# Kernel optimization log

Measured on AMD Instinct MI355X. Metric: run time of the kernel, lower is better.

## Reference

```python
import jax, jax.numpy as jnp
import numpy as np
import math

N_EMBD = 512
N_HEAD = 8
B, T = 2, 4096


def setup_inputs() -> dict:
    key = jax.random.key(0)
    ks = jax.random.split(key, 12)
    s = 1.0 / math.sqrt(N_EMBD)
    inp = {
        "x": jax.random.normal(ks[0], (B, T, N_EMBD), dtype=jnp.float32),
        "weight": jax.random.uniform(ks[1], (1,), dtype=jnp.float32),
        "state": jax.random.uniform(ks[2], (1,), dtype=jnp.float32),
        "Wq": jax.random.normal(ks[3], (N_EMBD, N_EMBD), dtype=jnp.float32) * s,
        "bq": jnp.zeros((N_EMBD,), dtype=jnp.float32),
        "Wk": jax.random.normal(ks[4], (N_EMBD, N_EMBD), dtype=jnp.float32) * s,
        "bk": jnp.zeros((N_EMBD,), dtype=jnp.float32),
        "Wv": jax.random.normal(ks[5], (N_EMBD, N_EMBD), dtype=jnp.float32) * s,
        "bv": jnp.zeros((N_EMBD,), dtype=jnp.float32),
        "Wp": jax.random.normal(ks[6], (N_EMBD, N_EMBD), dtype=jnp.float32) * s,
        "bp": jnp.zeros((N_EMBD,), dtype=jnp.float32),
    }
    return inp


def reference(x, weight, state, Wq, bq, Wk, bk, Wv, bv, Wp, bp):
    # weight / state are accepted but unused, matching the torch module.
    Bb, Tt, C = x.shape
    hd = C // N_HEAD

    def split_heads(t):  # [B,T,C] -> [B,H,T,hd]
        return t.reshape(Bb, Tt, N_HEAD, hd).transpose(0, 2, 1, 3)

    # torch nn.Linear: y = x @ W.T + b
    q = split_heads(x @ Wq.T + bq)
    k = split_heads(x @ Wk.T + bk)
    v = split_heads(x @ Wv.T + bv)

    scale = 1.0 / math.sqrt(hd)
    att = jnp.einsum("bhqd,bhkd->bhqk", q, k) * scale  # [B,H,T,T]
    causal = jnp.tril(jnp.ones((Tt, Tt), dtype=bool))
    att = jnp.where(causal[None, None, :, :], att, -jnp.inf)
    att = jax.nn.softmax(att, axis=-1)
    # attn_drop / resid_drop are identity (p=0 / eval)
    y = jnp.einsum("bhqk,bhkd->bhqd", att, v)  # [B,H,T,hd]
    y = y.transpose(0, 2, 1, 3).reshape(Bb, Tt, C)
    return y @ Wp.T + bp
```

## Files before the change

### kernel.cpp

```cpp
#include <hip/hip_runtime.h>
#include <math.h>

using short8  = __attribute__((ext_vector_type(8))) short;
using floatx4 = __attribute__((ext_vector_type(4))) float;

#define DEVI __device__ __forceinline__

#define BATCH 2
#define SEQ   4096
#define NE    512
#define NH    8
#define HD    64
#define MTOT  8192

#define QSCALE 0.18033688011112042f

DEVI short f2bf(float f) {
    unsigned u = __builtin_bit_cast(unsigned, f);
    unsigned r = (u + 0x7fffu + ((u >> 16) & 1u)) >> 16;
    return (short)r;
}

DEVI void async16(const void* g, void* l) {
    __builtin_amdgcn_global_load_lds(
        (const __attribute__((address_space(1))) void*)g,
        (__attribute__((address_space(3))) void*)l, 16, 0, 0);
}

__global__ __launch_bounds__(256) void cvt_all(const float* __restrict__ x,
                                               const float* __restrict__ wq,
                                               const float* __restrict__ wk,
                                               const float* __restrict__ wv,
                                               const float* __restrict__ wp,
                                               short* __restrict__ xbf,
                                               short* __restrict__ wbf) {
    int i = blockIdx.x * 256 + threadIdx.x;
    const float* src; short* dst; int off;
    if (i < MTOT * NE / 4) {
        src = x; dst = xbf; off = i;
    } else {
        int j = i - MTOT * NE / 4;
        int wsel = j >> 16;
        off = j & 65535;
        src = (wsel == 0) ? wq : (wsel == 1) ? wk : (wsel == 2) ? wv : wp;
        dst = wbf + (size_t)wsel * NE * NE;
    }
    float4 f = ((const float4*)src)[off];
    short4 o;
    o.x = f2bf(f.x); o.y = f2bf(f.y); o.z = f2bf(f.z); o.w = f2bf(f.w);
    ((short4*)dst)[off] = o;
}

DEVI void gemm_mainloop(const short* __restrict__ A, const short* __restrict__ W,
                        int m0, int n0, short* ldsA, short* ldsW, floatx4 (&acc)[4][4]) {
    const int tid  = threadIdx.x;
    const int lane = tid & 63;
    const int w    = tid >> 6;
    const int wm   = w >> 1, wn = w & 1;
    const int quad = lane >> 4, l15 = lane & 15;
    const int srow = lane >> 3, scol = (lane & 7) * 8;

    for (int i = 0; i < 4; ++i)
        for (int j = 0; j < 4; ++j)
            acc[i][j] = floatx4{0.f, 0.f, 0.f, 0.f};

    for (int kt = 0; kt < NE / 64; ++kt) {
        const int k0 = kt * 64;
        for (int c = 0; c < 4; ++c) {
            const int rb = w * 32 + c * 8;
            async16(A + (size_t)(m0 + rb + srow) * NE + k0 + scol, ldsA + rb * 64);
            async16(W + (size_t)(n0 + rb + srow) * NE + k0 + scol, ldsW + rb * 64);
        }
        __syncthreads();
        for (int ks = 0; ks < 2; ++ks) {
            short8 af[4], bf[4];
            for (int i = 0; i < 4; ++i)
                af[i] = *(const short8*)(ldsA + (wm * 64 + i * 16 + l15) * 64 + ks * 32 + quad * 8);
            for (int j = 0; j < 4; ++j)
                bf[j] = *(const short8*)(ldsW + (wn * 64 + j * 16 + l15) * 64 + ks * 32 + quad * 8);
            for (int i = 0; i < 4; ++i)
                for (int j = 0; j < 4; ++j)
                    acc[i][j] = __builtin_amdgcn_mfma_f32_16x16x32_bf16(af[i], bf[j], acc[i][j], 0, 0, 0);
        }
        __syncthreads();
    }
}

__global__ __launch_bounds__(256) void gemm_qkv(const short* __restrict__ xbf,
                                                const short* __restrict__ wbf,
                                                const float* __restrict__ bq,
                                                const float* __restrict__ bk,
                                                const float* __restrict__ bv,
                                                short* __restrict__ qkv) {
    __shared__ short ldsA[128 * 64];
    __shared__ short ldsW[128 * 64];
    const int m0 = blockIdx.x * 128, n0 = blockIdx.y * 128, z = blockIdx.z;
    const short* W = wbf + (size_t)z * (NE * NE);
    const float* bias = (z == 0) ? bq : (z == 1) ? bk : bv;
    short* out = qkv + (size_t)z * (MTOT * NE);

    floatx4 acc[4][4];
    gemm_mainloop(xbf, W, m0, n0, ldsA, ldsW, acc);

    const int lane = threadIdx.x & 63, w = threadIdx.x >> 6;
    const int wm = w >> 1, wn = w & 1, quad = lane >> 4, l15 = lane & 15;
    const float scale = (z == 0) ? QSCALE : 1.0f;
    for (int j = 0; j < 4; ++j) {
        const int col = n0 + wn * 64 + j * 16 + l15;
        const float bz = bias[col];
        const int h = col >> 6, d = col & 63;
        for (int i = 0; i < 4; ++i) {
            for (int r = 0; r < 4; ++r) {
                const int row = m0 + wm * 64 + i * 16 + quad * 4 + r;
                const int b = row >> 12, t = row & 4095;
                const float v = (acc[i][j][r] + bz) * scale;
                out[(((size_t)(b * NH + h)) * SEQ + t) * HD + d] = f2bf(v);
            }
        }
    }
}

__global__ __launch_bounds__(256) void transpose_v(const short* __restrict__ vb,
                                                   short* __restrict__ vt) {
    const int bh = blockIdx.y;
    const int t0 = blockIdx.x * 64;
    __shared__ short tile[64 * 66];
    const int tid = threadIdx.x;
    const int r  = tid >> 3;
    const int c8 = tid & 7;

    const short* src = vb + ((size_t)bh * SEQ + t0) * HD;
#pragma unroll
    for (int p = 0; p < 2; ++p) {
        const int row = p * 32 + r;
        short8 v = *(const short8*)&src[row * HD + c8 * 8];
#pragma unroll
        for (int i = 0; i < 8; ++i)
            tile[row * 66 + c8 * 8 + i] = v[i];
    }
    __syncthreads();

    short* dst = vt + (size_t)bh * (HD * SEQ) + t0;
#pragma unroll
    for (int p = 0; p < 2; ++p) {
        const int d = p * 32 + r;
        short8 o;
#pragma unroll
        for (int i = 0; i < 8; ++i)
            o[i] = tile[(c8 * 8 + i) * 66 + d];
        *(short8*)&dst[(size_t)d * SEQ + c8 * 8] = o;
    }
}

__global__ __launch_bounds__(256) void gemm_proj(const short* __restrict__ ybf,
                                                 const short* __restrict__ wp,
                                                 const float* __restrict__ bp,
                                                 float* __restrict__ out) {
    __shared__ short ldsA[128 * 64];
    __shared__ short ldsW[128 * 64];
    const int m0 = blockIdx.x * 128, n0 = blockIdx.y * 128;

    floatx4 acc[4][4];
    gemm_mainloop(ybf, wp, m0, n0, ldsA, ldsW, acc);

    const int lane = threadIdx.x & 63, w = threadIdx.x >> 6;
    const int wm = w >> 1, wn = w & 1, quad = lane >> 4, l15 = lane & 15;
    for (int j = 0; j < 4; ++j) {
        const int col = n0 + wn * 64 + j * 16 + l15;
        const float bz = bp[col];
        for (int i = 0; i < 4; ++i) {
            for (int r = 0; r < 4; ++r) {
                const int row = m0 + wm * 64 + i * 16 + quad * 4 + r;
                out[(size_t)row * NE + col] = acc[i][j][r] + bz;
            }
        }
    }
}

template<bool DOMASK>
DEVI void attn_subtile(const short* __restrict__ bK, const short* __restrict__ bV,
                       const short8 (&qfrag)[2], short* __restrict__ myP,
                       floatx4 (&O)[4], float (&lsum)[4],
                       const int p0, const int p1, const int quad, const int l15,
                       const int w) {
    short8 kf[2][4], vf[2][4];
#pragma unroll
    for (int n = 0; n < 4; ++n) {
        const int row = n * 16 + l15;
        kf[0][n] = *(const short8*)(bK + row * 64 + p0 * 8);
        kf[1][n] = *(const short8*)(bK + row * 64 + p1 * 8);
        vf[0][n] = *(const short8*)(bV + row * 64 + p0 * 8);
        vf[1][n] = *(const short8*)(bV + row * 64 + p1 * 8);
    }

    floatx4 S[4];
#pragma unroll
    for (int n = 0; n < 4; ++n) S[n] = floatx4{0.f, 0.f, 0.f, 0.f};
    __builtin_amdgcn_s_setprio(1);
#pragma unroll
    for (int ks = 0; ks < 2; ++ks)
#pragma unroll
        for (int n = 0; n < 4; ++n)
            S[n] = __builtin_amdgcn_mfma_f32_16x16x32_bf16(qfrag[ks], kf[ks][n], S[n], 0, 0, 0);
    __builtin_amdgcn_s_setprio(0);

    if (DOMASK) {
#pragma unroll
        for (int n = 0; n < 4; ++n)
#pragma unroll
            for (int r = 0; r < 4; ++r) {
                const int rowl = w * 16 + quad * 4 + r;
                const int coll = n * 16 + l15;
                if (coll > rowl) S[n][r] = -3.0e38f;
            }
    }

#pragma unroll
    for (int n = 0; n < 4; ++n)
#pragma unroll
        for (int r = 0; r < 4; ++r)
            S[n][r] = __builtin_amdgcn_exp2f(S[n][r]);
#pragma unroll
    for (int r = 0; r < 4; ++r)
        lsum[r] += (S[0][r] + S[1][r]) + (S[2][r] + S[3][r]);

#pragma unroll
    for (int n = 0; n < 4; ++n)
#pragma unroll
        for (int r = 0; r < 4; ++r)
            myP[(quad * 4 + r) * 72 + n * 16 + l15] = f2bf(S[n][r]);

    short8 pf[2];
#pragma unroll
    for (int ks = 0; ks < 2; ++ks)
        pf[ks] = *(const short8*)(myP + l15 * 72 + ks * 32 + quad * 8);

    __builtin_amdgcn_s_setprio(1);
#pragma unroll
    for (int ks = 0; ks < 2; ++ks)
#pragma unroll
        for (int n = 0; n < 4; ++n)
            O[n] = __builtin_amdgcn_mfma_f32_16x16x32_bf16(pf[ks], vf[ks][n], O[n], 0, 0, 0);
    __builtin_amdgcn_s_setprio(0);
}

__global__ __launch_bounds__(256, 2) void attn(const short* __restrict__ q,
                                               const short* __restrict__ k,
                                               const short* __restrict__ vt,
                                               short* __restrict__ y) {
    const int id = blockIdx.x;
    const int bx = id >> 4;
    const int bh = ((id & 7) << 1) | ((id >> 3) & 1);
    const int tid = threadIdx.x, lane = tid & 63, w = tid >> 6;
    const int quad = lane >> 4, l15 = lane & 15;

    __shared__ short ldsK[2][2][64 * 64];
    __shared__ short ldsV[2][2][64 * 64];
    __shared__ short ldsP[4][16 * 72];

    const short* K  = k  + (size_t)bh * (SEQ * HD);
    const short* VT = vt + (size_t)bh * (HD * SEQ);
    short* myP = (short*)ldsP[w];
    const int b = bh >> 3, h = bh & 7;

    const int lb   = ((lane & 7) - (lane >> 3)) & 7;
    const int jrow = lane >> 3;
    const int p0 = (quad + (l15 & 7)) & 7;
    const int p1 = p0 ^ 4;

    for (int sel = 0; sel < 2; ++sel) {
        const int qt = sel ? (SEQ / 64 - 1 - bx) : bx;
        const short* Q = q + (size_t)bh * (SEQ * HD) + (size_t)qt * 64 * HD;

        short8 qfrag[2];
#pragma unroll
        for (int ks = 0; ks < 2; ++ks)
            qfrag[ks] = *(const short8*)&Q[(w * 16 + l15) * HD + ks * 32 + quad * 8];

        floatx4 O[4];
        float lsum[4];
#pragma unroll
        for (int n = 0; n < 4; ++n) O[n] = floatx4{0.f, 0.f, 0.f, 0.f};
#pragma unroll
        for (int r = 0; r < 4; ++r) lsum[r] = 0.f;

        const int npair = (qt >> 1) + 1;

        __syncthreads();
#pragma unroll
        for (int s = 0; s < 2; ++s) {
            const short* Kt = K + (size_t)s * 64 * HD;
            const short* Vc = VT + s * 64;
#pragma unroll
            for (int c2 = 0; c2 < 2; ++c2) {
                const int chunk = w * 2 + c2;
                const int j = chunk * 8 + jrow;
                async16(Kt + (size_t)j * HD + lb * 8, ldsK[0][s] + chunk * 512);
                async16(Vc + (size_t)j * SEQ + lb * 8, ldsV[0][s] + chunk * 512);
            }
        }

        for (int p = 0; p + 1 < npair; ++p) {
            __syncthreads();
            const int pipe = p & 1, nx = pipe ^ 1;

#pragma unroll
            for (int s = 0; s < 2; ++s) {
                const int js = 2 * (p + 1) + s;
                const short* Kt = K + (size_t)js * 64 * HD;
                const short* Vc = VT + js * 64;
#pragma unroll
                for (int c2 = 0; c2 < 2; ++c2) {
                    const int chunk = w * 2 + c2;
                    const int j = chunk * 8 + jrow;
                    async16(Kt + (size_t)j * HD + lb * 8, ldsK[nx][s] + chunk * 512);
                    async16(Vc + (size_t)j * SEQ + lb * 8, ldsV[nx][s] + chunk * 512);
                }
            }

            attn_subtile<false>(ldsK[pipe][0], ldsV[pipe][0], qfrag, myP, O, lsum,
                                p0, p1, quad, l15, w);
            attn_subtile<false>(ldsK[pipe][1], ldsV[pipe][1], qfrag, myP, O, lsum,
                                p0, p1, quad, l15, w);
        }

        {
            __syncthreads();
            const int ep = (npair - 1) & 1;
            if (qt & 1) {
                attn_subtile<false>(ldsK[ep][0], ldsV[ep][0], qfrag, myP, O, lsum,
                                    p0, p1, quad, l15, w);
                attn_subtile<true >(ldsK[ep][1], ldsV[ep][1], qfrag, myP, O, lsum,
                                    p0, p1, quad, l15, w);
            } else {
                attn_subtile<true >(ldsK[ep][0], ldsV[ep][0], qfrag, myP, O, lsum,
                                    p0, p1, quad, l15, w);
            }
        }

#pragma unroll
        for (int r = 0; r < 4; ++r) {
#pragma unroll
            for (int off = 1; off < 16; off <<= 1)
                lsum[r] += __shfl_xor(lsum[r], off, 64);
        }

#pragma unroll
        for (int r = 0; r < 4; ++r) {
            const float inv = 1.0f / lsum[r];
            const int t = qt * 64 + w * 16 + quad * 4 + r;
#pragma unroll
            for (int n = 0; n < 4; ++n) {
                const int col = h * 64 + n * 16 + l15;
                y[((size_t)(b * SEQ + t)) * NE + col] = f2bf(O[n][r] * inv);
            }
        }
    }
}

extern "C" void kernel_launch(void* const* d_in, const int* in_sizes, int n_in,
                              void* d_out, int out_size, void* d_ws, size_t ws_size,
                              hipStream_t stream) {
    const float* x  = (const float*)d_in[0];
    const float* Wq = (const float*)d_in[3];
    const float* bq = (const float*)d_in[4];
    const float* Wk = (const float*)d_in[5];
    const float* bk = (const float*)d_in[6];
    const float* Wv = (const float*)d_in[7];
    const float* bv = (const float*)d_in[8];
    const float* Wp = (const float*)d_in[9];
    const float* bp = (const float*)d_in[10];
    float* out = (float*)d_out;

    short* ws   = (short*)d_ws;
    short* xbf  = ws;
    short* wbf  = xbf + (size_t)MTOT * NE;
    short* qb   = wbf + 4 * (size_t)NE * NE;
    short* kb   = qb + (size_t)MTOT * NE;
    short* vb   = kb + (size_t)MTOT * NE;
    short* vtb  = xbf;
    short* yb   = vb;

    cvt_all<<<dim3((MTOT * NE / 4 + 4 * NE * NE / 4) / 256), 256, 0, stream>>>(
        x, Wq, Wk, Wv, Wp, xbf, wbf);

    gemm_qkv<<<dim3(MTOT / 128, NE / 128, 3), 256, 0, stream>>>(xbf, wbf, bq, bk, bv, qb);

    transpose_v<<<dim3(SEQ / 64, BATCH * NH), 256, 0, stream>>>(vb, vtb);

    attn<<<dim3(512), 256, 0, stream>>>(qb, kb, vtb, yb);

    gemm_proj<<<dim3(MTOT / 128, NE / 128), 256, 0, stream>>>(yb, wbf + 3 * (size_t)NE * NE, bp, out);
}
```

Before: 204.0 us.

## Split attention work into one q-tile per block and read V directly from global

The attention kernel now launches one block per query tile (1024 blocks, longest tiles first) instead of pairing a short and long tile per block. V fragments are loaded straight from global memory rather than staged through LDS, which halves the shared-memory footprint and allows raising launch bounds to 3 blocks per CU. The aim is higher occupancy and better load balance, at the cost of uncoalesced, unpipelined global V loads and losing the explicit pairing balance.

```diff
diff --git a/kernel.cpp b/kernel.cpp
--- a/kernel.cpp
+++ b/kernel.cpp
@@ -178,19 +178,24 @@
 }
 
 template<bool DOMASK>
-DEVI void attn_subtile(const short* __restrict__ bK, const short* __restrict__ bV,
+DEVI void attn_subtile(const short* __restrict__ bK, const short* __restrict__ Vg,
                        const short8 (&qfrag)[2], short* __restrict__ myP,
                        floatx4 (&O)[4], float (&lsum)[4],
                        const int p0, const int p1, const int quad, const int l15,
                        const int w) {
-    short8 kf[2][4], vf[2][4];
+    short8 vf[2][4];
+#pragma unroll
+    for (int ks = 0; ks < 2; ++ks)
+#pragma unroll
+        for (int n = 0; n < 4; ++n)
+            vf[ks][n] = *(const short8*)&Vg[(size_t)(n * 16 + l15) * SEQ + ks * 32 + quad * 8];
+
+    short8 kf[2][4];
 #pragma unroll
     for (int n = 0; n < 4; ++n) {
         const int row = n * 16 + l15;
         kf[0][n] = *(const short8*)(bK + row * 64 + p0 * 8);
         kf[1][n] = *(const short8*)(bK + row * 64 + p1 * 8);
-        vf[0][n] = *(const short8*)(bV + row * 64 + p0 * 8);
-        vf[1][n] = *(const short8*)(bV + row * 64 + p1 * 8);
     }
 
     floatx4 S[4];
@@ -244,18 +249,17 @@
     __builtin_amdgcn_s_setprio(0);
 }
 
-__global__ __launch_bounds__(256, 2) void attn(const short* __restrict__ q,
+__global__ __launch_bounds__(256, 3) void attn(const short* __restrict__ q,
                                                const short* __restrict__ k,
                                                const short* __restrict__ vt,
                                                short* __restrict__ y) {
     const int id = blockIdx.x;
-    const int bx = id >> 4;
+    const int qt = 63 - (id >> 4);
     const int bh = ((id & 7) << 1) | ((id >> 3) & 1);
     const int tid = threadIdx.x, lane = tid & 63, w = tid >> 6;
     const int quad = lane >> 4, l15 = lane & 15;
 
     __shared__ short ldsK[2][2][64 * 64];
-    __shared__ short ldsV[2][2][64 * 64];
     __shared__ short ldsP[4][16 * 72];
 
     const short* K  = k  + (size_t)bh * (SEQ * HD);
@@ -268,92 +272,84 @@
     const int p0 = (quad + (l15 & 7)) & 7;
     const int p1 = p0 ^ 4;
 
-    for (int sel = 0; sel < 2; ++sel) {
-        const int qt = sel ? (SEQ / 64 - 1 - bx) : bx;
-        const short* Q = q + (size_t)bh * (SEQ * HD) + (size_t)qt * 64 * HD;
-
-        short8 qfrag[2];
-#pragma unroll
-        for (int ks = 0; ks < 2; ++ks)
-            qfrag[ks] = *(const short8*)&Q[(w * 16 + l15) * HD + ks * 32 + quad * 8];
-
-        floatx4 O[4];
-        float lsum[4];
-#pragma unroll
-        for (int n = 0; n < 4; ++n) O[n] = floatx4{0.f, 0.f, 0.f, 0.f};
-#pragma unroll
-        for (int r = 0; r < 4; ++r) lsum[r] = 0.f;
-
-        const int npair = (qt >> 1) + 1;
-
+    const short* Q = q + (size_t)bh * (SEQ * HD) + (size_t)qt * 64 * HD;
+
+    short8 qfrag[2];
+#pragma unroll
+    for (int ks = 0; ks < 2; ++ks)
+        qfrag[ks] = *(const short8*)&Q[(w * 16 + l15) * HD + ks * 32 + quad * 8];
+
+    floatx4 O[4];
+    float lsum[4];
+#pragma unroll
+    for (int n = 0; n < 4; ++n) O[n] = floatx4{0.f, 0.f, 0.f, 0.f};
+#pragma unroll
+    for (int r = 0; r < 4; ++r) lsum[r] = 0.f;
+
+    const int npair = (qt >> 1) + 1;
+
+#pragma unroll
+    for (int s = 0; s < 2; ++s) {
+        const short* Kt = K + (size_t)s * 64 * HD;
+#pragma unroll
+        for (int c2 = 0; c2 < 2; ++c2) {
+            const int chunk = w * 2 + c2;
+            const int j = chunk * 8 + jrow;
+            async16(Kt + (size_t)j * HD + lb * 8, ldsK[0][s] + chunk * 512);
+        }
+    }
+
+    for (int p = 0; p + 1 < npair; ++p) {
         __syncthreads();
+        const int pipe = p & 1, nx = pipe ^ 1;
+
 #pragma unroll
         for (int s = 0; s < 2; ++s) {
-            const short* Kt = K + (size_t)s * 64 * HD;
-            const short* Vc = VT + s * 64;
+            const int js = 2 * (p + 1) + s;
+            const short* Kt = K + (size_t)js * 64 * HD;
 #pragma unroll
             for (int c2 = 0; c2 < 2; ++c2) {
                 const int chunk = w * 2 + c2;
                 const int j = chunk * 8 + jrow;
-                async16(Kt + (size_t)j * HD + lb * 8, ldsK[0][s] + chunk * 512);
-                async16(Vc + (size_t)j * SEQ + lb * 8, ldsV[0][s] + chunk * 512);
+                async16(Kt + (size_t)j * HD + lb * 8, ldsK[nx][s] + chunk * 512);
             }
         }
 
-        for (int p = 0; p + 1 < npair; ++p) {
-            __syncthreads();
-            const int pipe = p & 1, nx = pipe ^ 1;
-
-#pragma unroll
-            for (int s = 0; s < 2; ++s) {
-                const int js = 2 * (p + 1) + s;
-                const short* Kt = K + (size_t)js * 64 * HD;
-                const short* Vc = VT + js * 64;
-#pragma unroll
-                for (int c2 = 0; c2 < 2; ++c2) {
-                    const int chunk = w * 2 + c2;
-                    const int j = chunk * 8 + jrow;
-                    async16(Kt + (size_t)j * HD + lb * 8, ldsK[nx][s] + chunk * 512);
-                    async16(Vc + (size_t)j * SEQ + lb * 8, ldsV[nx][s] + chunk * 512);
-                }
-            }
-
-            attn_subtile<false>(ldsK[pipe][0], ldsV[pipe][0], qfrag, myP, O, lsum,
+        attn_subtile<false>(ldsK[pipe][0], VT + (2 * p) * 64, qfrag, myP, O, lsum,
+                            p0, p1, quad, l15, w);
+        attn_subtile<false>(ldsK[pipe][1], VT + (2 * p + 1) * 64, qfrag, myP, O, lsum,
+                            p0, p1, quad, l15, w);
+    }
+
+    {
+        __syncthreads();
+        const int ep = (npair - 1) & 1;
+        if (qt & 1) {
+            attn_subtile<false>(ldsK[ep][0], VT + (qt - 1) * 64, qfrag, myP, O, lsum,
                                 p0, p1, quad, l15, w);
-            attn_subtile<false>(ldsK[pipe][1], ldsV[pipe][1], qfrag, myP, O, lsum,
+            attn_subtile<true >(ldsK[ep][1], VT + qt * 64, qfrag, myP, O, lsum,
                                 p0, p1, quad, l15, w);
-        }
-
-        {
-            __syncthreads();
-            const int ep = (npair - 1) & 1;
-            if (qt & 1) {
-                attn_subtile<false>(ldsK[ep][0], ldsV[ep][0], qfrag, myP, O, lsum,
-                                    p0, p1, quad, l15, w);
-                attn_subtile<true >(ldsK[ep][1], ldsV[ep][1], qfrag, myP, O, lsum,
-                                    p0, p1, quad, l15, w);
-            } else {
-                attn_subtile<true >(ldsK[ep][0], ldsV[ep][0], qfrag, myP, O, lsum,
-                                    p0, p1, quad, l15, w);
-            }
-        }
-
-#pragma unroll
-        for (int r = 0; r < 4; ++r) {
-#pragma unroll
-            for (int off = 1; off < 16; off <<= 1)
-                lsum[r] += __shfl_xor(lsum[r], off, 64);
-        }
-
-#pragma unroll
-        for (int r = 0; r < 4; ++r) {
-            const float inv = 1.0f / lsum[r];
-            const int t = qt * 64 + w * 16 + quad * 4 + r;
-#pragma unroll
-            for (int n = 0; n < 4; ++n) {
-                const int col = h * 64 + n * 16 + l15;
-                y[((size_t)(b * SEQ + t)) * NE + col] = f2bf(O[n][r] * inv);
-            }
+        } else {
+            attn_subtile<true >(ldsK[ep][0], VT + qt * 64, qfrag, myP, O, lsum,
+                                p0, p1, quad, l15, w);
+        }
+    }
+
+#pragma unroll
+    for (int r = 0; r < 4; ++r) {
+#pragma unroll
+        for (int off = 1; off < 16; off <<= 1)
+            lsum[r] += __shfl_xor(lsum[r], off, 64);
+    }
+
+#pragma unroll
+    for (int r = 0; r < 4; ++r) {
+        const float inv = 1.0f / lsum[r];
+        const int t = qt * 64 + w * 16 + quad * 4 + r;
+#pragma unroll
+        for (int n = 0; n < 4; ++n) {
+            const int col = h * 64 + n * 16 + l15;
+            y[((size_t)(b * SEQ + t)) * NE + col] = f2bf(O[n][r] * inv);
         }
     }
 }
@@ -388,7 +384,7 @@
 
     transpose_v<<<dim3(SEQ / 64, BATCH * NH), 256, 0, stream>>>(vb, vtb);
 
-    attn<<<dim3(512), 256, 0, stream>>>(qb, kb, vtb, yb);
+    attn<<<dim3(1024), 256, 0, stream>>>(qb, kb, vtb, yb);
 
     gemm_proj<<<dim3(MTOT / 128, NE / 128), 256, 0, stream>>>(yb, wbf + 3 * (size_t)NE * NE, bp, out);
 }
```

Result: slower. 273.8 us (+34.2%).
